# Kernel tuning notes

Measured on AMD Instinct MI355X. Metric: run time of the kernel, lower is better.

Reference implementation:

```python
import jax, jax.numpy as jnp
import numpy as np

S = 4        # support_num
NN = 32      # neighbor_num
BS, V = 2, 4096

def _normalize(x, axis):
    n = jnp.linalg.norm(x, axis=axis, keepdims=True)
    return x / jnp.maximum(n, 1e-12)

def _sqdist(a, b):
    aa = jnp.sum(a * a, -1)[:, :, None]
    bb = jnp.sum(b * b, -1)[:, None, :]
    return aa + bb - 2.0 * jnp.einsum('bnd,bmd->bnm', a, b)

def query_ball_point(radius, nsample, xyz, new_xyz):
    # PointNet++-style ball query: indices within radius, padded with first hit.
    N = xyz.shape[1]
    d2 = _sqdist(new_xyz, xyz)
    idx = jnp.broadcast_to(jnp.arange(N, dtype=jnp.int32), d2.shape)
    idx = jnp.where(d2 > radius * radius, N, idx)
    idx = jnp.sort(idx, axis=-1)[:, :, :nsample]
    first = idx[:, :, :1]
    return jnp.where(idx == N, jnp.broadcast_to(first, idx.shape), idx)

def _gather(feat, idx):
    # feat (B,N,C), idx (B,V,n) -> (B,V,n,C)
    return jax.vmap(lambda f, i: f[i])(feat, idx)

def _nbr_dir_norm(vertices, idx):
    nbr = _gather(vertices, idx)
    return _normalize(nbr - vertices[:, :, None, :], -1)

def conv_surface(idx, vertices, dirs, out_c):
    B, Vv, n = idx.shape
    nd = _nbr_dir_norm(vertices, idx)                             # (B,V,n,3)
    theta = jax.nn.relu(jnp.einsum('bvnd,dk->bvnk', nd, _normalize(dirs, 0)))
    theta = theta.reshape(B, Vv, n, S, out_c)
    return theta.max(axis=2).sum(axis=2)                          # (B,V,out)

def conv_layer(idx, vertices, fmap, W, b, dirs, out_c):
    B, Vv, n = idx.shape
    nd = _nbr_dir_norm(vertices, idx)
    theta = jax.nn.relu(jnp.einsum('bvnd,dk->bvnk', nd, _normalize(dirs, 0)))  # (B,V,n,S*out)
    fout = fmap @ W + b                                           # (B,V,(S+1)*out)
    center = fout[..., :out_c]
    support = _gather(fout[..., out_c:], idx)                     # (B,V,n,S*out)
    act = (theta * support).reshape(B, Vv, n, S, out_c).max(axis=2).sum(axis=2)
    return center + act

def pool(vertices, fmap, radius, key, rate=4, nnum=4):
    Vv = vertices.shape[1]
    idx = query_ball_point(radius, nnum, vertices, vertices)
    pooled = _gather(fmap, idx).max(axis=2)
    perm = jax.random.permutation(key, Vv)[: Vv // rate]
    return vertices[:, perm, :], pooled[:, perm, :]

def _forward(vertices, d0, w1, b1, dir1, w2, b2, dir2, w3, b3, dir3, w4, b4, dir4, w5, b5, dir5, w6, b6, dir6, w7, b7, dir7, w8, b8, dir8, cw1, cb1, bg, bb, cw2, cb2):
    idx = query_ball_point(0.2, NN, vertices, vertices)
    fm0 = jax.nn.relu(conv_surface(idx, vertices, d0, 32))
    fm1 = jax.nn.relu(conv_layer(idx, vertices, fm0, w1, b1, dir1, 32))
    fm1 = jnp.concatenate([fm0, fm1], 2)
    fm2 = jax.nn.relu(conv_layer(idx, vertices, fm1, w2, b2, dir2, 32))
    fm2 = jnp.concatenate([fm1, fm2], 2)
    vtx, fm2 = pool(vertices, fm2, 0.2, jax.random.key(1))
    idx = query_ball_point(0.4, NN, vtx, vtx)
    fm3 = jax.nn.relu(conv_layer(idx, vtx, fm2, w3, b3, dir3, 32))
    fm3 = jnp.concatenate([fm2, fm3], 2)
    fm4 = jax.nn.relu(conv_layer(idx, vtx, fm3, w4, b4, dir4, 32))
    fm4 = jnp.concatenate([fm3, fm4], 2)
    fm5 = jax.nn.relu(conv_layer(idx, vtx, fm4, w5, b5, dir5, 32))
    fm5 = jnp.concatenate([fm4, fm5], 2)
    vtx, fm5 = pool(vtx, fm5, 0.4, jax.random.key(2))
    idx = query_ball_point(0.6, NN, vtx, vtx)
    fm6 = jax.nn.relu(conv_layer(idx, vtx, fm5, w6, b6, dir6, 32))
    fm6 = jnp.concatenate([fm5, fm6], 2)
    fm7 = jax.nn.relu(conv_layer(idx, vtx, fm6, w7, b7, dir7, 32))
    fm7 = jnp.concatenate([fm6, fm7], 2)
    fm8 = conv_layer(idx, vtx, fm7, w8, b8, dir8, 1024)
    gfeat = fm8.max(axis=1)                                       # (B,1024)
    h = gfeat @ cw1 + cb1
    h = h / jnp.sqrt(1.0 + 1e-5) * bg + bb                        # BN1d eval (mean 0, var 1); dropout off
    h = jax.nn.relu(h)
    return h @ cw2 + cb2                                          # (B,40)

def setup_inputs() -> dict:
    key = jax.random.key(0)
    ks = iter(jax.random.split(key, 64))
    def nrm(shape, scale=0.1):
        return jax.random.normal(next(ks), shape, dtype=jnp.float32) * scale
    d = {}
    d['vertices'] = jax.random.uniform(next(ks), (BS, V, 3), dtype=jnp.float32)
    d['d0'] = nrm((3, S * 32))
    ins = [32, 64, 96, 128, 160, 192, 224, 256]
    outs = [32, 32, 32, 32, 32, 32, 32, 1024]
    for i, (ic, oc) in enumerate(zip(ins, outs), 1):
        d[f'w{i}'] = nrm((ic, (S + 1) * oc))
        d[f'b{i}'] = nrm(((S + 1) * oc,), 0.01)
        d[f'dir{i}'] = nrm((3, S * oc))
    d['cw1'] = nrm((1024, 256))
    d['cb1'] = nrm((256,), 0.01)
    d['bg'] = jnp.ones((256,), jnp.float32)
    d['bb'] = jnp.zeros((256,), jnp.float32)
    d['cw2'] = nrm((256, 40))
    d['cb2'] = nrm((40,), 0.01)
    return d

def reference(vertices, d0, w1, b1, dir1, w2, b2, dir2, w3, b3, dir3, w4, b4, dir4, w5, b5, dir5, w6, b6, dir6, w7, b7, dir7, w8, b8, dir8, cw1, cb1, bg, bb, cw2, cb2):
    return _forward(vertices, d0, w1, b1, dir1, w2, b2, dir2, w3, b3, dir3, w4, b4, dir4, w5, b5, dir5, w6, b6, dir6, w7, b7, dir7, w8, b8, dir8, cw1, cb1, bg, bb, cw2, cb2)
```

## Files before the change

### kernel.cpp

```cpp
#include <hip/hip_runtime.h>
#include <stdint.h>
#include <math.h>

#define NS 32

__device__ __forceinline__ void threefry(uint32_t k0, uint32_t k1,
                                         uint32_t x0, uint32_t x1,
                                         uint32_t& o0, uint32_t& o1)
{
    uint32_t ks0 = k0, ks1 = k1, ks2 = k0 ^ k1 ^ 0x1BD11BDAu;
    x0 += ks0; x1 += ks1;
    const int rotA[4] = {13, 15, 26, 6};
    const int rotB[4] = {17, 29, 16, 24};
    uint32_t ks[3] = {ks0, ks1, ks2};
#pragma unroll
    for (int i = 0; i < 5; ++i) {
        const int* r = (i & 1) ? rotB : rotA;
#pragma unroll
        for (int j = 0; j < 4; ++j) {
            x0 += x1;
            x1 = (x1 << r[j]) | (x1 >> (32 - r[j]));
            x1 ^= x0;
        }
        x0 += ks[(i + 1) % 3];
        x1 += ks[(i + 2) % 3] + (uint32_t)(i + 1);
    }
    o0 = x0; o1 = x1;
}

__global__ void perm_genkeys(uint32_t* __restrict__ keys, int* __restrict__ val,
                             uint32_t seed, int round, int n, int initval)
{
    int i = blockIdx.x * blockDim.x + threadIdx.x;
    if (i >= n) return;
    uint32_t k0 = 0u, k1 = seed;
    for (int r = 0; r < round; ++r) {
        uint32_t a0, a1;
        threefry(k0, k1, 0u, 0u, a0, a1);
        k0 = a0; k1 = a1;
    }
    uint32_t s0, s1;
    threefry(k0, k1, 0u, 1u, s0, s1);
    uint32_t y0, y1;
    threefry(s0, s1, 0u, (uint32_t)i, y0, y1);
    keys[i] = y0 ^ y1;
    if (initval) val[i] = i;
}

template <int N>
__global__ void perm_rank(const uint32_t* __restrict__ keys,
                          const int* __restrict__ vin, int* __restrict__ vout)
{
    __shared__ uint32_t sk[N];
    for (int j = threadIdx.x; j < N; j += blockDim.x) sk[j] = keys[j];
    __syncthreads();
    int w = threadIdx.x >> 6, lane = threadIdx.x & 63;
    int i = blockIdx.x * 4 + w;
    uint32_t k = sk[i];
    int c = 0;
    for (int j = lane; j < N; j += 64) {
        uint32_t kj = sk[j];
        c += (int)((kj < k) | ((kj == k) & (j < i)));
    }
#pragma unroll
    for (int m = 1; m < 64; m <<= 1) c += __shfl_xor(c, m, 64);
    if (lane == 0) vout[c] = vin[i];
}

__global__ void qbp_wave_kernel(const float* __restrict__ pts, int Vv, float r2,
                                int* __restrict__ idx, float* __restrict__ nd)
{
#pragma clang fp contract(off)
    int b = blockIdx.y;
    int v = blockIdx.x * 4 + (threadIdx.x >> 6);
    int lane = threadIdx.x & 63;
    if (v >= Vv) return;
    const float* P = pts + (size_t)b * Vv * 3;
    float qx = P[v * 3 + 0], qy = P[v * 3 + 1], qz = P[v * 3 + 2];
    float aa = (qx * qx + qy * qy) + qz * qz;
    int* orow = idx + ((size_t)b * Vv + v) * NS;
    float* nrow = nd + ((size_t)b * Vv + v) * NS * 3;
    int cnt = 0;
    int fj = 0; float fx = 0.f, fy = 0.f, fz = 0.f;
    bool have_first = false;
    for (int j0 = 0; j0 < Vv; j0 += 64) {
        int j = j0 + lane;
        float px = P[j * 3 + 0], py = P[j * 3 + 1], pz = P[j * 3 + 2];
        float bb2 = (px * px + py * py) + pz * pz;
        float dot = (qx * px + qy * py) + qz * pz;
        float d2 = (aa + bb2) - 2.0f * dot;
        bool in = (d2 <= r2);
        unsigned long long m = __ballot(in);
        if (m) {
            float dx = px - qx, dy = py - qy, dz = pz - qz;
            float nn = sqrtf((dx * dx + dy * dy) + dz * dz);
            float mm = fmaxf(nn, 1e-12f);
            float ndx = dx / mm, ndy = dy / mm, ndz = dz / mm;
            int rank = __popcll(m & ((1ULL << lane) - 1ULL));
            int pos = cnt + rank;
            if (in && pos < NS) {
                orow[pos] = j;
                nrow[pos * 3 + 0] = ndx;
                nrow[pos * 3 + 1] = ndy;
                nrow[pos * 3 + 2] = ndz;
            }
            if (!have_first) {
                int src = __ffsll((unsigned long long)m) - 1;
                fj = __shfl(j, src, 64);
                fx = __shfl(ndx, src, 64);
                fy = __shfl(ndy, src, 64);
                fz = __shfl(ndz, src, 64);
                have_first = true;
            }
            cnt += (int)__popcll(m);
            if (cnt >= NS) break;
        }
    }
    if (cnt < NS) {
        int k = cnt + lane;
        if (k < NS) {
            orow[k] = fj;
            nrow[k * 3 + 0] = fx; nrow[k * 3 + 1] = fy; nrow[k * 3 + 2] = fz;
        }
    }
}

__global__ void conv_surface_kernel(const float* __restrict__ nd, const float* __restrict__ dirs,
                                    float* __restrict__ fm, int Vv, int Cstr, int coff)
{
    __shared__ float snd[NS * 3];
    __shared__ float sm[128];
    int b = blockIdx.y, v = blockIdx.x, t = threadIdx.x;
    size_t row = (size_t)b * Vv + v;
    if (t < NS * 3) snd[t] = nd[row * NS * 3 + t];
    __syncthreads();
    float w0 = dirs[t], w1 = dirs[128 + t], w2 = dirs[256 + t];
    float nn = sqrtf(w0 * w0 + w1 * w1 + w2 * w2);
    float mm = fmaxf(nn, 1e-12f);
    w0 /= mm; w1 /= mm; w2 /= mm;
    float mx = -INFINITY;
#pragma unroll
    for (int n = 0; n < NS; ++n) {
        float th = fmaxf(snd[n * 3] * w0 + snd[n * 3 + 1] * w1 + snd[n * 3 + 2] * w2, 0.0f);
        mx = fmaxf(mx, th);
    }
    sm[t] = mx;
    __syncthreads();
    if (t < 32) {
        float o = ((sm[t] + sm[32 + t]) + sm[64 + t]) + sm[96 + t];
        o = fmaxf(o, 0.0f);
        fm[row * Cstr + coff + t] = o;
    }
}

__global__ void gemm_kernel(const float* __restrict__ A, const float* __restrict__ W,
                            const float* __restrict__ bias, float* __restrict__ C,
                            int K, int N, int lda)
{
    const int BM = 128, BN = 32, BK = 32;
    __shared__ float sA[BK][BM + 4];
    __shared__ float sB[BK][BN + 4];
    int t = threadIdx.x;
    int bm = blockIdx.y * BM, bn = blockIdx.x * BN;
    int tm = t & 31, tn = t >> 5;
    float acc[4][4] = {{0.f}};
    for (int k0 = 0; k0 < K; k0 += BK) {
#pragma unroll
        for (int i = 0; i < 4; ++i) {
            int q = t + i * 256;
            int m = q >> 3, kq = q & 7;
            float4 a = *(const float4*)&A[(size_t)(bm + m) * lda + k0 + kq * 4];
            sA[kq * 4 + 0][m] = a.x;
            sA[kq * 4 + 1][m] = a.y;
            sA[kq * 4 + 2][m] = a.z;
            sA[kq * 4 + 3][m] = a.w;
        }
        {
            int n4 = t & 7, k = t >> 3;
            float4 bv = *(const float4*)&W[(size_t)(k0 + k) * N + bn + n4 * 4];
            *(float4*)&sB[k][n4 * 4] = bv;
        }
        __syncthreads();
#pragma unroll
        for (int k = 0; k < BK; ++k) {
            float4 a4 = *(const float4*)&sA[k][tm * 4];
            float4 b4 = *(const float4*)&sB[k][tn * 4];
            float av[4] = {a4.x, a4.y, a4.z, a4.w};
            float bv[4] = {b4.x, b4.y, b4.z, b4.w};
#pragma unroll
            for (int i = 0; i < 4; ++i)
#pragma unroll
                for (int j = 0; j < 4; ++j)
                    acc[i][j] += av[i] * bv[j];
        }
        __syncthreads();
    }
    float4 bb = *(const float4*)&bias[bn + tn * 4];
    float bvv[4] = {bb.x, bb.y, bb.z, bb.w};
#pragma unroll
    for (int i = 0; i < 4; ++i) {
        float4 o;
        o.x = acc[i][0] + bvv[0];
        o.y = acc[i][1] + bvv[1];
        o.z = acc[i][2] + bvv[2];
        o.w = acc[i][3] + bvv[3];
        *(float4*)&C[(size_t)(bm + tm * 4 + i) * N + bn + tn * 4] = o;
    }
}

__global__ void act32_kernel(const float* __restrict__ nd, const int* __restrict__ idx,
                             const float* __restrict__ fout, const float* __restrict__ dirs,
                             float* __restrict__ fm, int Vv, int Cstr, int coff, int dorelu)
{
    __shared__ float snd[NS * 3];
    __shared__ int sidx[NS];
    __shared__ float sm[128];
    int b = blockIdx.y, v = blockIdx.x, t = threadIdx.x;
    size_t row = (size_t)b * Vv + v;
    if (t < NS * 3) snd[t] = nd[row * NS * 3 + t];
    if (t < NS) sidx[t] = idx[row * NS + t];
    __syncthreads();
    float w0 = dirs[t], w1 = dirs[128 + t], w2 = dirs[256 + t];
    float nn = sqrtf(w0 * w0 + w1 * w1 + w2 * w2);
    float mm = fmaxf(nn, 1e-12f);
    w0 /= mm; w1 /= mm; w2 /= mm;
    float mx = -INFINITY;
    for (int n = 0; n < NS; ++n) {
        float th = fmaxf(snd[n * 3] * w0 + snd[n * 3 + 1] * w1 + snd[n * 3 + 2] * w2, 0.0f);
        float sup = fout[((size_t)b * Vv + sidx[n]) * 160 + 32 + t];
        mx = fmaxf(mx, th * sup);
    }
    sm[t] = mx;
    __syncthreads();
    if (t < 32) {
        float act = ((sm[t] + sm[32 + t]) + sm[64 + t]) + sm[96 + t];
        float o = fout[row * 160 + t] + act;
        if (dorelu) o = fmaxf(o, 0.0f);
        fm[row * Cstr + coff + t] = o;
    }
}

__global__ void pool_kernel(const float* __restrict__ fmin, const int* __restrict__ idxp,
                            const int* __restrict__ perm, const float* __restrict__ vin,
                            float* __restrict__ fmout, float* __restrict__ vout,
                            int Vin, int Vout, int Cin, int Cout)
{
    int b = blockIdx.y, nv = blockIdx.x, t = threadIdx.x;
    int pv = perm[nv];
    size_t inrow = (size_t)b * Vin + pv;
    const int* ir = idxp + inrow * NS;
    int j0 = ir[0], j1 = ir[1], j2 = ir[2], j3 = ir[3];
    if (t < Cin) {
        const float* base = fmin + (size_t)b * Vin * Cin;
        float m = base[(size_t)j0 * Cin + t];
        m = fmaxf(m, base[(size_t)j1 * Cin + t]);
        m = fmaxf(m, base[(size_t)j2 * Cin + t]);
        m = fmaxf(m, base[(size_t)j3 * Cin + t]);
        fmout[((size_t)b * Vout + nv) * Cout + t] = m;
    }
    if (t == 0) {
        vout[((size_t)b * Vout + nv) * 3 + 0] = vin[inrow * 3 + 0];
        vout[((size_t)b * Vout + nv) * 3 + 1] = vin[inrow * 3 + 1];
        vout[((size_t)b * Vout + nv) * 3 + 2] = vin[inrow * 3 + 2];
    }
}

__global__ void act8_kernel(const float* __restrict__ nd, const int* __restrict__ idx,
                            const float* __restrict__ fout8, const float* __restrict__ dir8,
                            float* __restrict__ fm8)
{
    __shared__ float sdx[4096], sdy[4096], sdz[4096];
    __shared__ float snd[NS * 3];
    __shared__ int sidx[NS];
    int b = blockIdx.y, v = blockIdx.x, t = threadIdx.x;
    for (int c = t; c < 4096; c += 256) {
        float w0 = dir8[c], w1 = dir8[4096 + c], w2 = dir8[8192 + c];
        float nn = sqrtf(w0 * w0 + w1 * w1 + w2 * w2);
        float mm = fmaxf(nn, 1e-12f);
        sdx[c] = w0 / mm; sdy[c] = w1 / mm; sdz[c] = w2 / mm;
    }
    size_t row = (size_t)b * 256 + v;
    if (t < NS * 3) snd[t] = nd[row * NS * 3 + t];
    if (t < NS) sidx[t] = idx[row * NS + t];
    __syncthreads();
    float mx[16];
#pragma unroll
    for (int u = 0; u < 16; ++u) mx[u] = -INFINITY;
    for (int n = 0; n < NS; ++n) {
        float a0 = snd[n * 3], a1 = snd[n * 3 + 1], a2 = snd[n * 3 + 2];
        const float* sup = fout8 + ((size_t)b * 256 + sidx[n]) * 5120 + 1024;
#pragma unroll
        for (int u = 0; u < 16; ++u) {
            int k = t + 256 * u;
            float th = fmaxf(a0 * sdx[k] + a1 * sdy[k] + a2 * sdz[k], 0.0f);
            mx[u] = fmaxf(mx[u], th * sup[k]);
        }
    }
    const float* crow = fout8 + row * 5120;
#pragma unroll
    for (int w = 0; w < 4; ++w) {
        int c = t + 256 * w;
        float act = ((mx[w] + mx[4 + w]) + mx[8 + w]) + mx[12 + w];
        fm8[row * 1024 + c] = crow[c] + act;
    }
}

__global__ void gmax_part_kernel(const float* __restrict__ fm8, float* __restrict__ part)
{
    int cc = blockIdx.x, vc = blockIdx.y, b = blockIdx.z, t = threadIdx.x;
    int c = cc * 256 + t;
    float m = -INFINITY;
#pragma unroll 8
    for (int v = vc * 32; v < vc * 32 + 32; ++v)
        m = fmaxf(m, fm8[((size_t)b * 256 + v) * 1024 + c]);
    part[((size_t)b * 8 + vc) * 1024 + c] = m;
}

__global__ void gmax_final_kernel(const float* __restrict__ part, float* __restrict__ gfeat)
{
    int t = blockIdx.x * blockDim.x + threadIdx.x;
    if (t >= 2048) return;
    int b = t >> 10, c = t & 1023;
    float m = -INFINITY;
#pragma unroll
    for (int vc = 0; vc < 8; ++vc)
        m = fmaxf(m, part[((size_t)b * 8 + vc) * 1024 + c]);
    gfeat[t] = m;
}

__global__ void head1_kernel(const float* __restrict__ gfeat,
                             const float* __restrict__ cw1, const float* __restrict__ cb1,
                             const float* __restrict__ bg, const float* __restrict__ bbv,
                             float* __restrict__ h)
{
    __shared__ float sg[1024];
    __shared__ float sp[16][17];
    int b = blockIdx.y, c0 = blockIdx.x * 16, t = threadIdx.x;
    for (int i = t; i < 1024; i += 256) sg[i] = gfeat[b * 1024 + i];
    __syncthreads();
    int kg = t >> 4, cl = t & 15;
    float acc = 0.f;
#pragma unroll 8
    for (int i = 0; i < 64; ++i) {
        int k = kg * 64 + i;
        acc += sg[k] * cw1[k * 256 + c0 + cl];
    }
    sp[kg][cl] = acc;
    __syncthreads();
    if (t < 16) {
        float a = 0.f;
#pragma unroll
        for (int g = 0; g < 16; ++g) a += sp[g][t];
        int c = c0 + t;
        float hv = a + cb1[c];
        const float s = sqrtf((float)(1.0 + 1e-5));
        hv = hv / s * bg[c] + bbv[c];
        h[b * 256 + c] = fmaxf(hv, 0.0f);
    }
}

__global__ void head2_kernel(const float* __restrict__ h,
                             const float* __restrict__ cw2, const float* __restrict__ cb2,
                             float* __restrict__ out)
{
    __shared__ float sh[256];
    int b = blockIdx.x, t = threadIdx.x;
    sh[t] = h[b * 256 + t];
    __syncthreads();
    if (t < 40) {
        float a = 0.f;
        for (int i = 0; i < 256; ++i) a += sh[i] * cw2[i * 40 + t];
        out[b * 40 + t] = a + cb2[t];
    }
}

extern "C" void kernel_launch(void* const* d_in, const int* in_sizes, int n_in,
                              void* d_out, int out_size, void* d_ws, size_t ws_size,
                              hipStream_t stream)
{
    (void)in_sizes; (void)n_in; (void)out_size; (void)ws_size;
    const float* vertices = (const float*)d_in[0];
    const float* d0 = (const float*)d_in[1];
    const float *w[9], *bw[9], *dir[9];
    for (int i = 1; i <= 8; ++i) {
        w[i]   = (const float*)d_in[2 + (i - 1) * 3];
        bw[i]  = (const float*)d_in[3 + (i - 1) * 3];
        dir[i] = (const float*)d_in[4 + (i - 1) * 3];
    }
    const float* cw1 = (const float*)d_in[26];
    const float* cb1 = (const float*)d_in[27];
    const float* bg  = (const float*)d_in[28];
    const float* bbv = (const float*)d_in[29];
    const float* cw2 = (const float*)d_in[30];
    const float* cb2 = (const float*)d_in[31];
    float* out = (float*)d_out;

    char* ws = (char*)d_ws;
    size_t off = 0;
    auto take = [&](size_t bytes) -> char* {
        char* p = ws + off;
        off = (off + bytes + 255) & ~(size_t)255;
        return p;
    };
    uint32_t* keys1 = (uint32_t*)take(4096 * 4);
    int* valA = (int*)take(4096 * 4);
    int* valB = (int*)take(4096 * 4);
    uint32_t* keys2 = (uint32_t*)take(1024 * 4);
    int* v2A = (int*)take(1024 * 4);
    int* v2B = (int*)take(1024 * 4);
    int*   idx1 = (int*)take((size_t)2 * 4096 * NS * 4);
    float* nd1  = (float*)take((size_t)2 * 4096 * NS * 3 * 4);
    float* fmA  = (float*)take((size_t)2 * 4096 * 96 * 4);
    float* vtxB = (float*)take((size_t)2 * 1024 * 3 * 4);
    int*   idx2 = (int*)take((size_t)2 * 1024 * NS * 4);
    float* nd2  = (float*)take((size_t)2 * 1024 * NS * 3 * 4);
    float* fmB  = (float*)take((size_t)2 * 1024 * 192 * 4);
    float* vtxC = (float*)take((size_t)2 * 256 * 3 * 4);
    int*   idx3 = (int*)take((size_t)2 * 256 * NS * 4);
    float* nd3  = (float*)take((size_t)2 * 256 * NS * 3 * 4);
    float* fmC  = (float*)take((size_t)2 * 256 * 256 * 4);
    float* fm8  = (float*)take((size_t)2 * 256 * 1024 * 4);
    float* gpart = (float*)take((size_t)2 * 8 * 1024 * 4);
    float* gfeat = (float*)take(2 * 1024 * 4);
    float* hbuf  = (float*)take(2 * 256 * 4);
    float* fout = (float*)take((size_t)512 * 5120 * 4);

    perm_genkeys<<<16, 256, 0, stream>>>(keys1, valA, 1u, 0, 4096, 1);
    perm_rank<4096><<<1024, 256, 0, stream>>>(keys1, valA, valB);
    perm_genkeys<<<16, 256, 0, stream>>>(keys1, valA, 1u, 1, 4096, 0);
    perm_rank<4096><<<1024, 256, 0, stream>>>(keys1, valB, valA);
    perm_genkeys<<<4, 256, 0, stream>>>(keys2, v2A, 2u, 0, 1024, 1);
    perm_rank<1024><<<256, 256, 0, stream>>>(keys2, v2A, v2B);

    const float r2a = (float)(0.2 * 0.2), r2b = (float)(0.4 * 0.4), r2c = (float)(0.6 * 0.6);

    qbp_wave_kernel<<<dim3(1024, 2), 256, 0, stream>>>(vertices, 4096, r2a, idx1, nd1);
    conv_surface_kernel<<<dim3(4096, 2), 128, 0, stream>>>(nd1, d0, fmA, 4096, 96, 0);
    gemm_kernel<<<dim3(5, 64), 256, 0, stream>>>(fmA, w[1], bw[1], fout, 32, 160, 96);
    act32_kernel<<<dim3(4096, 2), 128, 0, stream>>>(nd1, idx1, fout, dir[1], fmA, 4096, 96, 32, 1);
    gemm_kernel<<<dim3(5, 64), 256, 0, stream>>>(fmA, w[2], bw[2], fout, 64, 160, 96);
    act32_kernel<<<dim3(4096, 2), 128, 0, stream>>>(nd1, idx1, fout, dir[2], fmA, 4096, 96, 64, 1);
    pool_kernel<<<dim3(1024, 2), 128, 0, stream>>>(fmA, idx1, valA, vertices, fmB, vtxB, 4096, 1024, 96, 192);

    qbp_wave_kernel<<<dim3(256, 2), 256, 0, stream>>>(vtxB, 1024, r2b, idx2, nd2);
    gemm_kernel<<<dim3(5, 16), 256, 0, stream>>>(fmB, w[3], bw[3], fout, 96, 160, 192);
    act32_kernel<<<dim3(1024, 2), 128, 0, stream>>>(nd2, idx2, fout, dir[3], fmB, 1024, 192, 96, 1);
    gemm_kernel<<<dim3(5, 16), 256, 0, stream>>>(fmB, w[4], bw[4], fout, 128, 160, 192);
    act32_kernel<<<dim3(1024, 2), 128, 0, stream>>>(nd2, idx2, fout, dir[4], fmB, 1024, 192, 128, 1);
    gemm_kernel<<<dim3(5, 16), 256, 0, stream>>>(fmB, w[5], bw[5], fout, 160, 160, 192);
    act32_kernel<<<dim3(1024, 2), 128, 0, stream>>>(nd2, idx2, fout, dir[5], fmB, 1024, 192, 160, 1);
    pool_kernel<<<dim3(256, 2), 256, 0, stream>>>(fmB, idx2, v2B, vtxB, fmC, vtxC, 1024, 256, 192, 256);

    qbp_wave_kernel<<<dim3(64, 2), 256, 0, stream>>>(vtxC, 256, r2c, idx3, nd3);
    gemm_kernel<<<dim3(5, 4), 256, 0, stream>>>(fmC, w[6], bw[6], fout, 192, 160, 256);
    act32_kernel<<<dim3(256, 2), 128, 0, stream>>>(nd3, idx3, fout, dir[6], fmC, 256, 256, 192, 1);
    gemm_kernel<<<dim3(5, 4), 256, 0, stream>>>(fmC, w[7], bw[7], fout, 224, 160, 256);
    act32_kernel<<<dim3(256, 2), 128, 0, stream>>>(nd3, idx3, fout, dir[7], fmC, 256, 256, 224, 1);

    gemm_kernel<<<dim3(160, 4), 256, 0, stream>>>(fmC, w[8], bw[8], fout, 256, 5120, 256);
    act8_kernel<<<dim3(256, 2), 256, 0, stream>>>(nd3, idx3, fout, dir[8], fm8);
    gmax_part_kernel<<<dim3(4, 8, 2), 256, 0, stream>>>(fm8, gpart);
    gmax_final_kernel<<<8, 256, 0, stream>>>(gpart, gfeat);
    head1_kernel<<<dim3(16, 2), 256, 0, stream>>>(gfeat, cw1, cb1, bg, bbv, hbuf);
    head2_kernel<<<2, 256, 0, stream>>>(hbuf, cw2, cb2, out);
}
```

Baseline: 276.1 us.

## Merge permutation launches, use one wave per vertex, split act8 across blocks, fuse gmax

The permutation key generation is merged into one launch, and two of the rank passes are combined into a single dual-job launch, cutting the launch count. The conv_surface and act32 kernels now give each vertex one 64-lane wave, four vertices per block, and finish the support reduction with a shuffle instead of shared memory and a second barrier. act8 is split over a z-grid of 4 channel quarters, which raises parallelism and shrinks its shared-memory footprint. The gmax_final kernel is folded into head1, which now reduces the partial maxima itself.

```diff
diff --git a/kernel.cpp b/kernel.cpp
--- a/kernel.cpp
+++ b/kernel.cpp
@@ -28,11 +28,8 @@
     o0 = x0; o1 = x1;
 }
 
-__global__ void perm_genkeys(uint32_t* __restrict__ keys, int* __restrict__ val,
-                             uint32_t seed, int round, int n, int initval)
-{
-    int i = blockIdx.x * blockDim.x + threadIdx.x;
-    if (i >= n) return;
+__device__ __forceinline__ uint32_t perm_key(uint32_t seed, int round, uint32_t i)
+{
     uint32_t k0 = 0u, k1 = seed;
     for (int r = 0; r < round; ++r) {
         uint32_t a0, a1;
@@ -42,9 +39,27 @@
     uint32_t s0, s1;
     threefry(k0, k1, 0u, 1u, s0, s1);
     uint32_t y0, y1;
-    threefry(s0, s1, 0u, (uint32_t)i, y0, y1);
-    keys[i] = y0 ^ y1;
-    if (initval) val[i] = i;
+    threefry(s0, s1, 0u, i, y0, y1);
+    return y0 ^ y1;
+}
+
+__global__ void perm_genkeys_all(uint32_t* __restrict__ keys1, uint32_t* __restrict__ keys1b,
+                                 uint32_t* __restrict__ keys2,
+                                 int* __restrict__ valA, int* __restrict__ v2A)
+{
+    int blk = blockIdx.x, t = threadIdx.x;
+    if (blk < 16) {
+        int i = blk * 256 + t;
+        keys1[i] = perm_key(1u, 0, (uint32_t)i);
+        valA[i] = i;
+    } else if (blk < 32) {
+        int i = (blk - 16) * 256 + t;
+        keys1b[i] = perm_key(1u, 1, (uint32_t)i);
+    } else {
+        int i = (blk - 32) * 256 + t;
+        keys2[i] = perm_key(2u, 0, (uint32_t)i);
+        v2A[i] = i;
+    }
 }
 
 template <int N>
@@ -56,6 +71,33 @@
     __syncthreads();
     int w = threadIdx.x >> 6, lane = threadIdx.x & 63;
     int i = blockIdx.x * 4 + w;
+    uint32_t k = sk[i];
+    int c = 0;
+    for (int j = lane; j < N; j += 64) {
+        uint32_t kj = sk[j];
+        c += (int)((kj < k) | ((kj == k) & (j < i)));
+    }
+#pragma unroll
+    for (int m = 1; m < 64; m <<= 1) c += __shfl_xor(c, m, 64);
+    if (lane == 0) vout[c] = vin[i];
+}
+
+__global__ void perm_rank_dual(const uint32_t* __restrict__ kA, const int* __restrict__ vinA,
+                               int* __restrict__ voutA,
+                               const uint32_t* __restrict__ kB, const int* __restrict__ vinB,
+                               int* __restrict__ voutB)
+{
+    __shared__ uint32_t sk[4096];
+    bool jobB = (blockIdx.x >= 1024);
+    const uint32_t* keys = jobB ? kB : kA;
+    const int* vin = jobB ? vinB : vinA;
+    int* vout = jobB ? voutB : voutA;
+    int N = jobB ? 1024 : 4096;
+    int base = jobB ? (blockIdx.x - 1024) : blockIdx.x;
+    for (int j = threadIdx.x; j < N; j += blockDim.x) sk[j] = keys[j];
+    __syncthreads();
+    int w = threadIdx.x >> 6, lane = threadIdx.x & 63;
+    int i = base * 4 + w;
     uint32_t k = sk[i];
     int c = 0;
     for (int j = lane; j < N; j += 64) {
@@ -125,32 +167,37 @@
     }
 }
 
-__global__ void conv_surface_kernel(const float* __restrict__ nd, const float* __restrict__ dirs,
-                                    float* __restrict__ fm, int Vv, int Cstr, int coff)
-{
-    __shared__ float snd[NS * 3];
-    __shared__ float sm[128];
-    int b = blockIdx.y, v = blockIdx.x, t = threadIdx.x;
+__global__ void conv_surface_wave(const float* __restrict__ nd, const float* __restrict__ dirs,
+                                  float* __restrict__ fm, int Vv, int Cstr, int coff)
+{
+    __shared__ float snd[4][96];
+    int b = blockIdx.y, t = threadIdx.x;
+    int wid = t >> 6, lane = t & 63;
+    int v = blockIdx.x * 4 + wid;
     size_t row = (size_t)b * Vv + v;
-    if (t < NS * 3) snd[t] = nd[row * NS * 3 + t];
-    __syncthreads();
-    float w0 = dirs[t], w1 = dirs[128 + t], w2 = dirs[256 + t];
-    float nn = sqrtf(w0 * w0 + w1 * w1 + w2 * w2);
-    float mm = fmaxf(nn, 1e-12f);
-    w0 /= mm; w1 /= mm; w2 /= mm;
-    float mx = -INFINITY;
+    const float* src = nd + row * NS * 3;
+    snd[wid][lane] = src[lane];
+    if (lane < 32) snd[wid][64 + lane] = src[64 + lane];
+    __syncthreads();
+    int c = lane & 31, sh = lane >> 5;
+    int t1 = sh * 32 + c, t2 = t1 + 64;
+    float w0a = dirs[t1], w1a = dirs[128 + t1], w2a = dirs[256 + t1];
+    float w0b = dirs[t2], w1b = dirs[128 + t2], w2b = dirs[256 + t2];
+    float na = fmaxf(sqrtf(w0a * w0a + w1a * w1a + w2a * w2a), 1e-12f);
+    float nb = fmaxf(sqrtf(w0b * w0b + w1b * w1b + w2b * w2b), 1e-12f);
+    w0a /= na; w1a /= na; w2a /= na;
+    w0b /= nb; w1b /= nb; w2b /= nb;
+    float mx1 = -INFINITY, mx2 = -INFINITY;
 #pragma unroll
     for (int n = 0; n < NS; ++n) {
-        float th = fmaxf(snd[n * 3] * w0 + snd[n * 3 + 1] * w1 + snd[n * 3 + 2] * w2, 0.0f);
-        mx = fmaxf(mx, th);
-    }
-    sm[t] = mx;
-    __syncthreads();
-    if (t < 32) {
-        float o = ((sm[t] + sm[32 + t]) + sm[64 + t]) + sm[96 + t];
-        o = fmaxf(o, 0.0f);
-        fm[row * Cstr + coff + t] = o;
-    }
+        float a0 = snd[wid][n * 3], a1 = snd[wid][n * 3 + 1], a2 = snd[wid][n * 3 + 2];
+        mx1 = fmaxf(mx1, fmaxf(a0 * w0a + a1 * w1a + a2 * w2a, 0.0f));
+        mx2 = fmaxf(mx2, fmaxf(a0 * w0b + a1 * w1b + a2 * w2b, 0.0f));
+    }
+    float sum = mx1 + mx2;
+    sum += __shfl_xor(sum, 32, 64);
+    if (sh == 0)
+        fm[row * Cstr + coff + c] = fmaxf(sum, 0.0f);
 }
 
 __global__ void gemm_kernel(const float* __restrict__ A, const float* __restrict__ W,
@@ -208,35 +255,46 @@
     }
 }
 
-__global__ void act32_kernel(const float* __restrict__ nd, const int* __restrict__ idx,
-                             const float* __restrict__ fout, const float* __restrict__ dirs,
-                             float* __restrict__ fm, int Vv, int Cstr, int coff, int dorelu)
-{
-    __shared__ float snd[NS * 3];
-    __shared__ int sidx[NS];
-    __shared__ float sm[128];
-    int b = blockIdx.y, v = blockIdx.x, t = threadIdx.x;
+__global__ void act32_wave(const float* __restrict__ nd, const int* __restrict__ idx,
+                           const float* __restrict__ fout, const float* __restrict__ dirs,
+                           float* __restrict__ fm, int Vv, int Cstr, int coff, int dorelu)
+{
+    __shared__ float snd[4][96];
+    __shared__ int sidx[4][32];
+    int b = blockIdx.y, t = threadIdx.x;
+    int wid = t >> 6, lane = t & 63;
+    int v = blockIdx.x * 4 + wid;
     size_t row = (size_t)b * Vv + v;
-    if (t < NS * 3) snd[t] = nd[row * NS * 3 + t];
-    if (t < NS) sidx[t] = idx[row * NS + t];
-    __syncthreads();
-    float w0 = dirs[t], w1 = dirs[128 + t], w2 = dirs[256 + t];
-    float nn = sqrtf(w0 * w0 + w1 * w1 + w2 * w2);
-    float mm = fmaxf(nn, 1e-12f);
-    w0 /= mm; w1 /= mm; w2 /= mm;
-    float mx = -INFINITY;
+    const float* src = nd + row * NS * 3;
+    const int* irow = idx + row * NS;
+    snd[wid][lane] = src[lane];
+    if (lane < 32) snd[wid][64 + lane] = src[64 + lane];
+    else sidx[wid][lane - 32] = irow[lane - 32];
+    __syncthreads();
+    int c = lane & 31, sh = lane >> 5;
+    int t1 = sh * 32 + c, t2 = t1 + 64;
+    float w0a = dirs[t1], w1a = dirs[128 + t1], w2a = dirs[256 + t1];
+    float w0b = dirs[t2], w1b = dirs[128 + t2], w2b = dirs[256 + t2];
+    float na = fmaxf(sqrtf(w0a * w0a + w1a * w1a + w2a * w2a), 1e-12f);
+    float nb = fmaxf(sqrtf(w0b * w0b + w1b * w1b + w2b * w2b), 1e-12f);
+    w0a /= na; w1a /= na; w2a /= na;
+    w0b /= nb; w1b /= nb; w2b /= nb;
+    const float* fb = fout + (size_t)b * Vv * 160;
+    float mx1 = -INFINITY, mx2 = -INFINITY;
     for (int n = 0; n < NS; ++n) {
-        float th = fmaxf(snd[n * 3] * w0 + snd[n * 3 + 1] * w1 + snd[n * 3 + 2] * w2, 0.0f);
-        float sup = fout[((size_t)b * Vv + sidx[n]) * 160 + 32 + t];
-        mx = fmaxf(mx, th * sup);
-    }
-    sm[t] = mx;
-    __syncthreads();
-    if (t < 32) {
-        float act = ((sm[t] + sm[32 + t]) + sm[64 + t]) + sm[96 + t];
-        float o = fout[row * 160 + t] + act;
+        float a0 = snd[wid][n * 3], a1 = snd[wid][n * 3 + 1], a2 = snd[wid][n * 3 + 2];
+        const float* sup = fb + (size_t)sidx[wid][n] * 160 + 32;
+        float th1 = fmaxf(a0 * w0a + a1 * w1a + a2 * w2a, 0.0f);
+        float th2 = fmaxf(a0 * w0b + a1 * w1b + a2 * w2b, 0.0f);
+        mx1 = fmaxf(mx1, th1 * sup[t1]);
+        mx2 = fmaxf(mx2, th2 * sup[t2]);
+    }
+    float sum = mx1 + mx2;
+    sum += __shfl_xor(sum, 32, 64);
+    if (sh == 0) {
+        float o = fout[row * 160 + c] + sum;
         if (dorelu) o = fmaxf(o, 0.0f);
-        fm[row * Cstr + coff + t] = o;
+        fm[row * Cstr + coff + c] = o;
     }
 }
 
@@ -269,40 +327,34 @@
                             const float* __restrict__ fout8, const float* __restrict__ dir8,
                             float* __restrict__ fm8)
 {
-    __shared__ float sdx[4096], sdy[4096], sdz[4096];
-    __shared__ float snd[NS * 3];
-    __shared__ int sidx[NS];
-    int b = blockIdx.y, v = blockIdx.x, t = threadIdx.x;
-    for (int c = t; c < 4096; c += 256) {
-        float w0 = dir8[c], w1 = dir8[4096 + c], w2 = dir8[8192 + c];
-        float nn = sqrtf(w0 * w0 + w1 * w1 + w2 * w2);
-        float mm = fmaxf(nn, 1e-12f);
-        sdx[c] = w0 / mm; sdy[c] = w1 / mm; sdz[c] = w2 / mm;
+    __shared__ float sd0[4][256], sd1[4][256], sd2[4][256];
+    __shared__ float snd[96];
+    __shared__ int sidx[32];
+    int v = blockIdx.x, b = blockIdx.y, wq = blockIdx.z, t = threadIdx.x;
+#pragma unroll
+    for (int j = 0; j < 4; ++j) {
+        int k = t + 256 * wq + 1024 * j;
+        float w0 = dir8[k], w1 = dir8[4096 + k], w2 = dir8[8192 + k];
+        float mm = fmaxf(sqrtf(w0 * w0 + w1 * w1 + w2 * w2), 1e-12f);
+        sd0[j][t] = w0 / mm; sd1[j][t] = w1 / mm; sd2[j][t] = w2 / mm;
     }
     size_t row = (size_t)b * 256 + v;
-    if (t < NS * 3) snd[t] = nd[row * NS * 3 + t];
-    if (t < NS) sidx[t] = idx[row * NS + t];
-    __syncthreads();
-    float mx[16];
-#pragma unroll
-    for (int u = 0; u < 16; ++u) mx[u] = -INFINITY;
+    if (t < 96) snd[t] = nd[row * NS * 3 + t];
+    else if (t < 128) sidx[t - 96] = idx[row * NS + t - 96];
+    __syncthreads();
+    float mx[4] = {-INFINITY, -INFINITY, -INFINITY, -INFINITY};
     for (int n = 0; n < NS; ++n) {
         float a0 = snd[n * 3], a1 = snd[n * 3 + 1], a2 = snd[n * 3 + 2];
-        const float* sup = fout8 + ((size_t)b * 256 + sidx[n]) * 5120 + 1024;
-#pragma unroll
-        for (int u = 0; u < 16; ++u) {
-            int k = t + 256 * u;
-            float th = fmaxf(a0 * sdx[k] + a1 * sdy[k] + a2 * sdz[k], 0.0f);
-            mx[u] = fmaxf(mx[u], th * sup[k]);
-        }
-    }
-    const float* crow = fout8 + row * 5120;
-#pragma unroll
-    for (int w = 0; w < 4; ++w) {
-        int c = t + 256 * w;
-        float act = ((mx[w] + mx[4 + w]) + mx[8 + w]) + mx[12 + w];
-        fm8[row * 1024 + c] = crow[c] + act;
-    }
+        const float* sup = fout8 + ((size_t)b * 256 + sidx[n]) * 5120 + 1024 + 256 * wq;
+#pragma unroll
+        for (int j = 0; j < 4; ++j) {
+            float th = fmaxf(a0 * sd0[j][t] + a1 * sd1[j][t] + a2 * sd2[j][t], 0.0f);
+            mx[j] = fmaxf(mx[j], th * sup[t + 1024 * j]);
+        }
+    }
+    int c = t + 256 * wq;
+    float act = ((mx[0] + mx[1]) + mx[2]) + mx[3];
+    fm8[row * 1024 + c] = fout8[row * 5120 + c] + act;
 }
 
 __global__ void gmax_part_kernel(const float* __restrict__ fm8, float* __restrict__ part)
@@ -316,19 +368,7 @@
     part[((size_t)b * 8 + vc) * 1024 + c] = m;
 }
 
-__global__ void gmax_final_kernel(const float* __restrict__ part, float* __restrict__ gfeat)
-{
-    int t = blockIdx.x * blockDim.x + threadIdx.x;
-    if (t >= 2048) return;
-    int b = t >> 10, c = t & 1023;
-    float m = -INFINITY;
-#pragma unroll
-    for (int vc = 0; vc < 8; ++vc)
-        m = fmaxf(m, part[((size_t)b * 8 + vc) * 1024 + c]);
-    gfeat[t] = m;
-}
-
-__global__ void head1_kernel(const float* __restrict__ gfeat,
+__global__ void head1_kernel(const float* __restrict__ gpart,
                              const float* __restrict__ cw1, const float* __restrict__ cb1,
                              const float* __restrict__ bg, const float* __restrict__ bbv,
                              float* __restrict__ h)
@@ -336,7 +376,13 @@
     __shared__ float sg[1024];
     __shared__ float sp[16][17];
     int b = blockIdx.y, c0 = blockIdx.x * 16, t = threadIdx.x;
-    for (int i = t; i < 1024; i += 256) sg[i] = gfeat[b * 1024 + i];
+    for (int i = t; i < 1024; i += 256) {
+        float m = -INFINITY;
+#pragma unroll
+        for (int vc = 0; vc < 8; ++vc)
+            m = fmaxf(m, gpart[((size_t)b * 8 + vc) * 1024 + i]);
+        sg[i] = m;
+    }
     __syncthreads();
     int kg = t >> 4, cl = t & 15;
     float acc = 0.f;
@@ -402,7 +448,8 @@
         off = (off + bytes + 255) & ~(size_t)255;
         return p;
     };
-    uint32_t* keys1 = (uint32_t*)take(4096 * 4);
+    uint32_t* keys1  = (uint32_t*)take(4096 * 4);
+    uint32_t* keys1b = (uint32_t*)take(4096 * 4);
     int* valA = (int*)take(4096 * 4);
     int* valB = (int*)take(4096 * 4);
     uint32_t* keys2 = (uint32_t*)take(1024 * 4);
@@ -421,46 +468,41 @@
     float* fmC  = (float*)take((size_t)2 * 256 * 256 * 4);
     float* fm8  = (float*)take((size_t)2 * 256 * 1024 * 4);
     float* gpart = (float*)take((size_t)2 * 8 * 1024 * 4);
-    float* gfeat = (float*)take(2 * 1024 * 4);
     float* hbuf  = (float*)take(2 * 256 * 4);
     float* fout = (float*)take((size_t)512 * 5120 * 4);
 
-    perm_genkeys<<<16, 256, 0, stream>>>(keys1, valA, 1u, 0, 4096, 1);
-    perm_rank<4096><<<1024, 256, 0, stream>>>(keys1, valA, valB);
-    perm_genkeys<<<16, 256, 0, stream>>>(keys1, valA, 1u, 1, 4096, 0);
-    perm_rank<4096><<<1024, 256, 0, stream>>>(keys1, valB, valA);
-    perm_genkeys<<<4, 256, 0, stream>>>(keys2, v2A, 2u, 0, 1024, 1);
-    perm_rank<1024><<<256, 256, 0, stream>>>(keys2, v2A, v2B);
+    perm_genkeys_all<<<36, 256, 0, stream>>>(keys1, keys1b, keys2, valA, v2A);
+    perm_rank_dual<<<1280, 256, 0, stream>>>(keys1, valA, valB, keys2, v2A, v2B);
+    perm_rank<4096><<<1024, 256, 0, stream>>>(keys1b, valB, valA);
 
     const float r2a = (float)(0.2 * 0.2), r2b = (float)(0.4 * 0.4), r2c = (float)(0.6 * 0.6);
 
     qbp_wave_kernel<<<dim3(1024, 2), 256, 0, stream>>>(vertices, 4096, r2a, idx1, nd1);
-    conv_surface_kernel<<<dim3(4096, 2), 128, 0, stream>>>(nd1, d0, fmA, 4096, 96, 0);
+    conv_surface_wave<<<dim3(1024, 2), 256, 0, stream>>>(nd1, d0, fmA, 4096, 96, 0);
     gemm_kernel<<<dim3(5, 64), 256, 0, stream>>>(fmA, w[1], bw[1], fout, 32, 160, 96);
-    act32_kernel<<<dim3(4096, 2), 128, 0, stream>>>(nd1, idx1, fout, dir[1], fmA, 4096, 96, 32, 1);
+    act32_wave<<<dim3(1024, 2), 256, 0, stream>>>(nd1, idx1, fout, dir[1], fmA, 4096, 96, 32, 1);
     gemm_kernel<<<dim3(5, 64), 256, 0, stream>>>(fmA, w[2], bw[2], fout, 64, 160, 96);
-    act32_kernel<<<dim3(4096, 2), 128, 0, stream>>>(nd1, idx1, fout, dir[2], fmA, 4096, 96, 64, 1);
+    act32_wave<<<dim3(1024, 2), 256, 0, stream>>>(nd1, idx1, fout, dir[2], fmA, 4096, 96, 64, 1);
     pool_kernel<<<dim3(1024, 2), 128, 0, stream>>>(fmA, idx1, valA, vertices, fmB, vtxB, 4096, 1024, 96, 192);
 
     qbp_wave_kernel<<<dim3(256, 2), 256, 0, stream>>>(vtxB, 1024, r2b, idx2, nd2);
     gemm_kernel<<<dim3(5, 16), 256, 0, stream>>>(fmB, w[3], bw[3], fout, 96, 160, 192);
-    act32_kernel<<<dim3(1024, 2), 128, 0, stream>>>(nd2, idx2, fout, dir[3], fmB, 1024, 192, 96, 1);
+    act32_wave<<<dim3(256, 2), 256, 0, stream>>>(nd2, idx2, fout, dir[3], fmB, 1024, 192, 96, 1);
     gemm_kernel<<<dim3(5, 16), 256, 0, stream>>>(fmB, w[4], bw[4], fout, 128, 160, 192);
-    act32_kernel<<<dim3(1024, 2), 128, 0, stream>>>(nd2, idx2, fout, dir[4], fmB, 1024, 192, 128, 1);
+    act32_wave<<<dim3(256, 2), 256, 0, stream>>>(nd2, idx2, fout, dir[4], fmB, 1024, 192, 128, 1);
     gemm_kernel<<<dim3(5, 16), 256, 0, stream>>>(fmB, w[5], bw[5], fout, 160, 160, 192);
-    act32_kernel<<<dim3(1024, 2), 128, 0, stream>>>(nd2, idx2, fout, dir[5], fmB, 1024, 192, 160, 1);
+    act32_wave<<<dim3(256, 2), 256, 0, stream>>>(nd2, idx2, fout, dir[5], fmB, 1024, 192, 160, 1);
     pool_kernel<<<dim3(256, 2), 256, 0, stream>>>(fmB, idx2, v2B, vtxB, fmC, vtxC, 1024, 256, 192, 256);
 
     qbp_wave_kernel<<<dim3(64, 2), 256, 0, stream>>>(vtxC, 256, r2c, idx3, nd3);
     gemm_kernel<<<dim3(5, 4), 256, 0, stream>>>(fmC, w[6], bw[6], fout, 192, 160, 256);
-    act32_kernel<<<dim3(256, 2), 128, 0, stream>>>(nd3, idx3, fout, dir[6], fmC, 256, 256, 192, 1);
+    act32_wave<<<dim3(64, 2), 256, 0, stream>>>(nd3, idx3, fout, dir[6], fmC, 256, 256, 192, 1);
     gemm_kernel<<<dim3(5, 4), 256, 0, stream>>>(fmC, w[7], bw[7], fout, 224, 160, 256);
-    act32_kernel<<<dim3(256, 2), 128, 0, stream>>>(nd3, idx3, fout, dir[7], fmC, 256, 256, 224, 1);
+    act32_wave<<<dim3(64, 2), 256, 0, stream>>>(nd3, idx3, fout, dir[7], fmC, 256, 256, 224, 1);
 
     gemm_kernel<<<dim3(160, 4), 256, 0, stream>>>(fmC, w[8], bw[8], fout, 256, 5120, 256);
-    act8_kernel<<<dim3(256, 2), 256, 0, stream>>>(nd3, idx3, fout, dir[8], fm8);
+    act8_kernel<<<dim3(256, 2, 4), 256, 0, stream>>>(nd3, idx3, fout, dir[8], fm8);
     gmax_part_kernel<<<dim3(4, 8, 2), 256, 0, stream>>>(fm8, gpart);
-    gmax_final_kernel<<<8, 256, 0, stream>>>(gpart, gfeat);
-    head1_kernel<<<dim3(16, 2), 256, 0, stream>>>(gfeat, cw1, cb1, bg, bbv, hbuf);
+    head1_kernel<<<dim3(16, 2), 256, 0, stream>>>(gpart, cw1, cb1, bg, bbv, hbuf);
     head2_kernel<<<2, 256, 0, stream>>>(hbuf, cw2, cb2, out);
 }
```

Result: slower. 284.7 us (+3.1%).
